# Optimization experiments

Measured on AMD Instinct MI355X. Metric: run time of the kernel, lower is better.

## Reference

```python
import jax, jax.numpy as jnp
import numpy as np
import math

B, L, C_IN = 64, 3168, 64
D_MODEL, K = 512, 16  # K = cycle_length (kernel width == stride)
W = L // K            # 198 output tokens from deform conv


def _positional(S, d, dtype):
    # PositionalEmbedding buffer, rows [0, S)
    pos = jnp.arange(S, dtype=jnp.float32)[:, None]
    div = jnp.exp(jnp.arange(0, d, 2, dtype=jnp.float32) * (-math.log(10000.0) / d))
    pe = jnp.zeros((S, d), jnp.float32)
    pe = pe.at[:, 0::2].set(jnp.sin(pos * div))
    pe = pe.at[:, 1::2].set(jnp.cos(pos * div))
    return pe.astype(dtype)


def setup_inputs() -> dict:
    key = jax.random.key(0)
    ks = jax.random.split(key, 6)
    fan_in = C_IN * K
    std = math.sqrt(2.0 / (1 + 0.01 ** 2) / fan_in)  # kaiming_normal, leaky_relu fan_in
    return {
        "x": jax.random.normal(ks[0], (B, L, C_IN), jnp.float32),
        "w_off": jax.random.normal(ks[1], (2 * K, C_IN, K), jnp.float32) * std,
        "b_off": jax.random.normal(ks[2], (2 * K,), jnp.float32) * 0.02,
        "w_def": jax.random.normal(ks[3], (D_MODEL, C_IN, K), jnp.float32) * std,
        "b_def": jax.random.normal(ks[4], (D_MODEL,), jnp.float32) * 0.02,
        "cls_token": jax.random.normal(ks[5], (1, 1, D_MODEL), jnp.float32),
    }


def _gather_cols(xt, idx, L_):
    # xt: (B, C, L); idx: (B, K, W) int32 -> (B, C, K, W), zero out-of-bounds
    b, c = xt.shape[0], xt.shape[1]
    valid = (idx >= 0) & (idx < L_)
    idxc = jnp.clip(idx, 0, L_ - 1).reshape(b, 1, -1)
    g = jnp.take_along_axis(xt, jnp.broadcast_to(idxc, (b, c, idxc.shape[-1])), axis=2)
    g = g.reshape(b, c, idx.shape[1], idx.shape[2])
    return jnp.where(valid[:, None], g, 0.0)


def reference(x, w_off, b_off, w_def, b_def, cls_token):
    b, l, c = x.shape
    w = l // K
    # offset conv: kernel (1,K), stride (1,K) == non-overlapping windows
    xr = x[:, : w * K, :].reshape(b, w, K, c)              # (B, W, K, C)
    off = jnp.einsum('bwkc,ock->bow', xr, w_off) + b_off[None, :, None]  # (B, 2K, W)
    dy = off[:, 0::2]                                      # (B, K, W)
    dx = off[:, 1::2]
    # sampling positions along width (height is size 1, base y = 0)
    base = (jnp.arange(w)[None, :] * K + jnp.arange(K)[:, None]).astype(x.dtype)  # (K, W)
    px = base[None] + dx                                   # (B, K, W)
    x0 = jnp.floor(px)
    frac = px - x0
    x0i = x0.astype(jnp.int32)
    xt = x.transpose(0, 2, 1)                              # (B, C, L)
    v0 = _gather_cols(xt, x0i, l)
    v1 = _gather_cols(xt, x0i + 1, l)
    wy = jnp.maximum(0.0, 1.0 - jnp.abs(dy))               # vertical bilinear weight on row 0
    val = wy[:, None] * ((1.0 - frac)[:, None] * v0 + frac[:, None] * v1)  # (B, C, K, W)
    out = jnp.einsum('bckw,dck->bwd', val, w_def) + b_def  # (B, W, d_model)
    tok = jnp.concatenate([jnp.broadcast_to(cls_token, (b, 1, D_MODEL)), out], axis=1)
    pe = _positional(w + 1, D_MODEL, tok.dtype)
    return tok + pe[None]
```

## Files before the change

### kernel.cpp

```cpp
#include <hip/hip_runtime.h>
#include <math.h>
#include <stdint.h>

#define NB 64
#define NL 3168
#define NC 64
#define ND 512
#define NK 16
#define NW 198
#define NM 12672
#define KD 1024

typedef __attribute__((ext_vector_type(8))) short bf8_t;
typedef __attribute__((ext_vector_type(4))) float f4_t;

typedef const unsigned int __attribute__((address_space(1)))* as1_u32p;
typedef unsigned int __attribute__((address_space(3)))* as3_u32p;

__device__ __forceinline__ void gl_lds16(const void* g, void* l) {
  __builtin_amdgcn_global_load_lds((as1_u32p)(uintptr_t)g,
                                   (as3_u32p)(unsigned int)(uintptr_t)l, 16, 0, 0);
}

__device__ __forceinline__ unsigned short f2bf(float f) {
  union { float f; unsigned u; } v; v.f = f;
  unsigned r = v.u + 0x7FFFu + ((v.u >> 16) & 1u);
  return (unsigned short)(r >> 16);
}

__global__ void prep_kernel(const float* __restrict__ w_off, const float* __restrict__ w_def,
                            const float* __restrict__ cls, unsigned short* __restrict__ wofft,
                            unsigned short* __restrict__ wdeft, float* __restrict__ pe,
                            float* __restrict__ out) {
  int id = blockIdx.x * 256 + threadIdx.x;
  if (id < 524288) {
    int d = id >> 10, kc = id & 1023, k = kc >> 6, c = kc & 63;
    wdeft[id] = f2bf(w_def[d * 1024 + c * 16 + k]);
    return;
  }
  id -= 524288;
  if (id < 32768) {
    int o = id >> 10, kc = id & 1023, k = kc >> 6, c = kc & 63;
    wofft[id] = f2bf(w_off[o * 1024 + c * 16 + k]);
    return;
  }
  id -= 32768;
  if (id < 101888) {
    int pos = id >> 9, d = id & 511;
    int i = d >> 1;
    float freq = expf((float)(2 * i) * (-9.210340371976184f / 512.0f));
    float arg = (float)pos * freq;
    pe[id] = (d & 1) ? cosf(arg) : sinf(arg);
    return;
  }
  id -= 101888;
  {
    int b = id >> 9, d = id & 511;
    out[(size_t)(b * 199) * 512 + d] = cls[d] + ((d & 1) ? 1.0f : 0.0f);
  }
}

__launch_bounds__(256)
__global__ void offgemm_kernel(const float* __restrict__ x, const unsigned short* __restrict__ wofft,
                               const float* __restrict__ b_off, float* __restrict__ off_ws) {
  __shared__ float partial[4][16][33];
  int tid = threadIdx.x;
  int lane = tid & 63, wid = tid >> 6;
  int r16 = lane & 15, kg = lane >> 4;
  int row0 = blockIdx.x * 16;

  f4_t acc[2] = {};
  const float* arow = x + (size_t)(row0 + r16) * KD + wid * 256;
  const unsigned short* bcol0 = wofft + r16 * KD + wid * 256;
  const unsigned short* bcol1 = wofft + (16 + r16) * KD + wid * 256;

#pragma unroll
  for (int ks = 0; ks < 8; ++ks) {
    int k0 = ks * 32 + kg * 8;
    float4 v0 = *(const float4*)(arow + k0);
    float4 v1 = *(const float4*)(arow + k0 + 4);
    bf8_t a;
    a[0] = (short)f2bf(v0.x); a[1] = (short)f2bf(v0.y);
    a[2] = (short)f2bf(v0.z); a[3] = (short)f2bf(v0.w);
    a[4] = (short)f2bf(v1.x); a[5] = (short)f2bf(v1.y);
    a[6] = (short)f2bf(v1.z); a[7] = (short)f2bf(v1.w);
    bf8_t b0 = *(const bf8_t*)(bcol0 + k0);
    bf8_t b1 = *(const bf8_t*)(bcol1 + k0);
    acc[0] = __builtin_amdgcn_mfma_f32_16x16x32_bf16(a, b0, acc[0], 0, 0, 0);
    acc[1] = __builtin_amdgcn_mfma_f32_16x16x32_bf16(a, b1, acc[1], 0, 0, 0);
  }
#pragma unroll
  for (int n = 0; n < 2; ++n)
#pragma unroll
    for (int r = 0; r < 4; ++r)
      partial[wid][kg * 4 + r][n * 16 + r16] = acc[n][r];
  __syncthreads();
#pragma unroll
  for (int i = 0; i < 2; ++i) {
    int idx = tid * 2 + i;
    int r = idx >> 5, o = idx & 31;
    float s = partial[0][r][o] + partial[1][r][o] + partial[2][r][o] + partial[3][r][o];
    off_ws[(row0 + r) * 32 + o] = s + b_off[o];
  }
}

__global__ void sample_kernel(const float* __restrict__ x, const float* __restrict__ off_ws,
                              unsigned short* __restrict__ val_ws) {
  int tid = threadIdx.x;
  int wid = tid >> 6, lane = tid & 63;
  int row = blockIdx.x * 4 + wid;
  int b = row / NW, w = row - b * NW;
  const float* xb = x + (size_t)b * (NL * NC);
  const float* offr = off_ws + row * 32;
  unsigned short* dst = val_ws + (size_t)row * KD;
#pragma unroll
  for (int k = 0; k < 16; ++k) {
    float dy = offr[2 * k], dx = offr[2 * k + 1];
    float wy = fmaxf(0.f, 1.f - fabsf(dy));
    float px = (float)(w * 16 + k) + dx;
    float x0f = floorf(px);
    float frac = px - x0f;
    int x0 = (int)x0f;
    float v0 = (x0 >= 0 && x0 < NL) ? xb[x0 * 64 + lane] : 0.f;
    float v1 = (x0 + 1 >= 0 && x0 + 1 < NL) ? xb[(x0 + 1) * 64 + lane] : 0.f;
    float val = wy * ((1.f - frac) * v0 + frac * v1);
    dst[k * 64 + lane] = f2bf(val);
  }
}

__launch_bounds__(256)
__global__ void gemm_kernel(const unsigned short* __restrict__ val_ws,
                            const unsigned short* __restrict__ wdeft,
                            const float* __restrict__ b_def, const float* __restrict__ pe,
                            float* __restrict__ out) {
  __shared__ unsigned short As[128 * 64];
  __shared__ unsigned short Bs[128 * 64];
  int tid = threadIdx.x;
  int mt = blockIdx.x, nt = blockIdx.y;
  int lane = tid & 63, wid = tid >> 6;
  int r16 = lane & 15, kg = lane >> 4;
  int wr = wid >> 1, wc = wid & 1;
  f4_t acc[4][4] = {};

  int r_st = lane >> 3;
  int j_st = lane & 7;
  const char* aBase = (const char*)val_ws + (size_t)mt * 128 * 2048;
  const char* bBase = (const char*)wdeft + (size_t)nt * 128 * 2048;

  for (int ks = 0; ks < 16; ++ks) {
    __syncthreads();
#pragma unroll
    for (int i = 0; i < 4; ++i) {
      int seg = wid * 4 + i;
      int r = seg * 8 + r_st;
      int src_off = ((j_st ^ (r & 7)) << 4);
      gl_lds16(aBase + (size_t)r * 2048 + ks * 128 + src_off, &As[seg * 512]);
      gl_lds16(bBase + (size_t)r * 2048 + ks * 128 + src_off, &Bs[seg * 512]);
    }
    __syncthreads();
#pragma unroll
    for (int jb = 0; jb < 8; jb += 4) {
      bf8_t af[4], bf[4];
#pragma unroll
      for (int m = 0; m < 4; ++m) {
        int R = wr * 64 + m * 16 + r16;
        af[m] = *(const bf8_t*)&As[R * 64 + (((jb + kg) ^ (R & 7)) << 3)];
      }
#pragma unroll
      for (int n = 0; n < 4; ++n) {
        int Rc = wc * 64 + n * 16 + r16;
        bf[n] = *(const bf8_t*)&Bs[Rc * 64 + (((jb + kg) ^ (Rc & 7)) << 3)];
      }
#pragma unroll
      for (int m = 0; m < 4; ++m)
#pragma unroll
        for (int n = 0; n < 4; ++n)
          acc[m][n] = __builtin_amdgcn_mfma_f32_16x16x32_bf16(af[m], bf[n], acc[m][n], 0, 0, 0);
    }
  }
#pragma unroll
  for (int m = 0; m < 4; ++m)
#pragma unroll
    for (int n = 0; n < 4; ++n)
#pragma unroll
      for (int r = 0; r < 4; ++r) {
        int grow = mt * 128 + wr * 64 + m * 16 + kg * 4 + r;
        int gcol = nt * 128 + wc * 64 + n * 16 + r16;
        int bi = grow / NW, wi = grow - bi * NW;
        out[((size_t)(bi * 199 + wi + 1)) * 512 + gcol] =
            acc[m][n][r] + b_def[gcol] + pe[(wi + 1) * 512 + gcol];
      }
}

extern "C" void kernel_launch(void* const* d_in, const int* in_sizes, int n_in,
                              void* d_out, int out_size, void* d_ws, size_t ws_size,
                              hipStream_t stream) {
  const float* x     = (const float*)d_in[0];
  const float* w_off = (const float*)d_in[1];
  const float* b_off = (const float*)d_in[2];
  const float* w_def = (const float*)d_in[3];
  const float* b_def = (const float*)d_in[4];
  const float* cls   = (const float*)d_in[5];
  float* out = (float*)d_out;
  char* ws = (char*)d_ws;
  unsigned short* val_ws = (unsigned short*)ws;
  unsigned short* wofft  = (unsigned short*)(ws + 25952256);
  unsigned short* wdeft  = (unsigned short*)(ws + 26017792);
  float* pe              = (float*)(ws + 27066368);
  float* off_ws          = (float*)(ws + 27473920);

  prep_kernel<<<2702, 256, 0, stream>>>(w_off, w_def, cls, wofft, wdeft, pe, out);
  offgemm_kernel<<<NM / 16, 256, 0, stream>>>(x, wofft, b_off, off_ws);
  sample_kernel<<<NM / 4, 256, 0, stream>>>(x, off_ws, val_ws);
  gemm_kernel<<<dim3(99, 4), 256, 0, stream>>>(val_ws, wdeft, b_def, pe, out);
}
```

Baseline: 68.28 us.

## Fuse offset GEMM with sampling, switch val layout to c-major, double-buffer GEMM

Merges the offset-conv GEMM and the bilinear sampling into one kernel. Offsets stay in shared memory instead of taking a round trip through global memory, and one launch is removed. Each lane now writes its 16 k-values contiguously with vector stores, so val and w_def use a (c,k) K-ordering and w_def can be converted without a transpose. The main GEMM gains double-buffered LDS staging with one barrier per step, so loads overlap MFMA work. The cost is fewer sampling threads per block and twice the LDS, which may lower occupancy.

```diff
diff --git a/kernel.cpp b/kernel.cpp
--- a/kernel.cpp
+++ b/kernel.cpp
@@ -34,8 +34,7 @@
                             float* __restrict__ out) {
   int id = blockIdx.x * 256 + threadIdx.x;
   if (id < 524288) {
-    int d = id >> 10, kc = id & 1023, k = kc >> 6, c = kc & 63;
-    wdeft[id] = f2bf(w_def[d * 1024 + c * 16 + k]);
+    wdeft[id] = f2bf(w_def[id]);
     return;
   }
   id -= 524288;
@@ -61,9 +60,12 @@
 }
 
 __launch_bounds__(256)
-__global__ void offgemm_kernel(const float* __restrict__ x, const unsigned short* __restrict__ wofft,
-                               const float* __restrict__ b_off, float* __restrict__ off_ws) {
+__global__ void offsample_kernel(const float* __restrict__ x,
+                                 const unsigned short* __restrict__ wofft,
+                                 const float* __restrict__ b_off,
+                                 unsigned short* __restrict__ val_ws) {
   __shared__ float partial[4][16][33];
+  __shared__ float offs[16][32];
   int tid = threadIdx.x;
   int lane = tid & 63, wid = tid >> 6;
   int r16 = lane & 15, kg = lane >> 4;
@@ -99,32 +101,37 @@
   for (int i = 0; i < 2; ++i) {
     int idx = tid * 2 + i;
     int r = idx >> 5, o = idx & 31;
-    float s = partial[0][r][o] + partial[1][r][o] + partial[2][r][o] + partial[3][r][o];
-    off_ws[(row0 + r) * 32 + o] = s + b_off[o];
-  }
-}
-
-__global__ void sample_kernel(const float* __restrict__ x, const float* __restrict__ off_ws,
-                              unsigned short* __restrict__ val_ws) {
-  int tid = threadIdx.x;
-  int wid = tid >> 6, lane = tid & 63;
-  int row = blockIdx.x * 4 + wid;
-  int b = row / NW, w = row - b * NW;
-  const float* xb = x + (size_t)b * (NL * NC);
-  const float* offr = off_ws + row * 32;
-  unsigned short* dst = val_ws + (size_t)row * KD;
-#pragma unroll
-  for (int k = 0; k < 16; ++k) {
-    float dy = offr[2 * k], dx = offr[2 * k + 1];
-    float wy = fmaxf(0.f, 1.f - fabsf(dy));
-    float px = (float)(w * 16 + k) + dx;
-    float x0f = floorf(px);
-    float frac = px - x0f;
-    int x0 = (int)x0f;
-    float v0 = (x0 >= 0 && x0 < NL) ? xb[x0 * 64 + lane] : 0.f;
-    float v1 = (x0 + 1 >= 0 && x0 + 1 < NL) ? xb[(x0 + 1) * 64 + lane] : 0.f;
-    float val = wy * ((1.f - frac) * v0 + frac * v1);
-    dst[k * 64 + lane] = f2bf(val);
+    offs[r][o] = partial[0][r][o] + partial[1][r][o] + partial[2][r][o] + partial[3][r][o]
+                 + b_off[o];
+  }
+  __syncthreads();
+
+#pragma unroll
+  for (int rr = 0; rr < 4; ++rr) {
+    int rp = wid * 4 + rr;
+    int rg = row0 + rp;
+    int b = rg / NW, w = rg - b * NW;
+    const float* xb = x + (size_t)b * (NL * NC);
+    unsigned short vv[16];
+#pragma unroll
+    for (int k = 0; k < 16; ++k) {
+      float dy = offs[rp][2 * k], dx = offs[rp][2 * k + 1];
+      float wy = fmaxf(0.f, 1.f - fabsf(dy));
+      float px = (float)(w * 16 + k) + dx;
+      float x0f = floorf(px);
+      float frac = px - x0f;
+      int x0 = (int)x0f;
+      float v0 = (x0 >= 0 && x0 < NL) ? xb[x0 * 64 + lane] : 0.f;
+      float v1 = (x0 + 1 >= 0 && x0 + 1 < NL) ? xb[(x0 + 1) * 64 + lane] : 0.f;
+      vv[k] = f2bf(wy * ((1.f - frac) * v0 + frac * v1));
+    }
+    unsigned int p[8];
+#pragma unroll
+    for (int i = 0; i < 8; ++i)
+      p[i] = (unsigned int)vv[2 * i] | ((unsigned int)vv[2 * i + 1] << 16);
+    uint4* dst = (uint4*)(val_ws + (size_t)rg * KD + lane * 16);
+    dst[0] = make_uint4(p[0], p[1], p[2], p[3]);
+    dst[1] = make_uint4(p[4], p[5], p[6], p[7]);
   }
 }
 
@@ -133,8 +140,8 @@
                             const unsigned short* __restrict__ wdeft,
                             const float* __restrict__ b_def, const float* __restrict__ pe,
                             float* __restrict__ out) {
-  __shared__ unsigned short As[128 * 64];
-  __shared__ unsigned short Bs[128 * 64];
+  __shared__ unsigned short As[2][128 * 64];
+  __shared__ unsigned short Bs[2][128 * 64];
   int tid = threadIdx.x;
   int mt = blockIdx.x, nt = blockIdx.y;
   int lane = tid & 63, wid = tid >> 6;
@@ -147,29 +154,30 @@
   const char* aBase = (const char*)val_ws + (size_t)mt * 128 * 2048;
   const char* bBase = (const char*)wdeft + (size_t)nt * 128 * 2048;
 
-  for (int ks = 0; ks < 16; ++ks) {
-    __syncthreads();
+  auto STAGE = [&](int ks, int buf) {
 #pragma unroll
     for (int i = 0; i < 4; ++i) {
       int seg = wid * 4 + i;
       int r = seg * 8 + r_st;
       int src_off = ((j_st ^ (r & 7)) << 4);
-      gl_lds16(aBase + (size_t)r * 2048 + ks * 128 + src_off, &As[seg * 512]);
-      gl_lds16(bBase + (size_t)r * 2048 + ks * 128 + src_off, &Bs[seg * 512]);
+      gl_lds16(aBase + (size_t)r * 2048 + ks * 128 + src_off, &As[buf][seg * 512]);
+      gl_lds16(bBase + (size_t)r * 2048 + ks * 128 + src_off, &Bs[buf][seg * 512]);
     }
-    __syncthreads();
+  };
+
+  auto COMPUTE = [&](int buf) {
 #pragma unroll
     for (int jb = 0; jb < 8; jb += 4) {
       bf8_t af[4], bf[4];
 #pragma unroll
       for (int m = 0; m < 4; ++m) {
         int R = wr * 64 + m * 16 + r16;
-        af[m] = *(const bf8_t*)&As[R * 64 + (((jb + kg) ^ (R & 7)) << 3)];
+        af[m] = *(const bf8_t*)&As[buf][R * 64 + (((jb + kg) ^ (R & 7)) << 3)];
       }
 #pragma unroll
       for (int n = 0; n < 4; ++n) {
         int Rc = wc * 64 + n * 16 + r16;
-        bf[n] = *(const bf8_t*)&Bs[Rc * 64 + (((jb + kg) ^ (Rc & 7)) << 3)];
+        bf[n] = *(const bf8_t*)&Bs[buf][Rc * 64 + (((jb + kg) ^ (Rc & 7)) << 3)];
       }
 #pragma unroll
       for (int m = 0; m < 4; ++m)
@@ -177,7 +185,18 @@
         for (int n = 0; n < 4; ++n)
           acc[m][n] = __builtin_amdgcn_mfma_f32_16x16x32_bf16(af[m], bf[n], acc[m][n], 0, 0, 0);
     }
-  }
+  };
+
+  STAGE(0, 0);
+  __syncthreads();
+#pragma unroll
+  for (int ks = 0; ks < 15; ++ks) {
+    STAGE(ks + 1, (ks + 1) & 1);
+    COMPUTE(ks & 1);
+    __syncthreads();
+  }
+  COMPUTE(1);
+
 #pragma unroll
   for (int m = 0; m < 4; ++m)
 #pragma unroll
@@ -207,10 +226,8 @@
   unsigned short* wofft  = (unsigned short*)(ws + 25952256);
   unsigned short* wdeft  = (unsigned short*)(ws + 26017792);
   float* pe              = (float*)(ws + 27066368);
-  float* off_ws          = (float*)(ws + 27473920);
 
   prep_kernel<<<2702, 256, 0, stream>>>(w_off, w_def, cls, wofft, wdeft, pe, out);
-  offgemm_kernel<<<NM / 16, 256, 0, stream>>>(x, wofft, b_off, off_ws);
-  sample_kernel<<<NM / 4, 256, 0, stream>>>(x, off_ws, val_ws);
+  offsample_kernel<<<NM / 16, 256, 0, stream>>>(x, wofft, b_off, val_ws);
   gemm_kernel<<<dim3(99, 4), 256, 0, stream>>>(val_ws, wdeft, b_def, pe, out);
 }
```

New measurement: 70.09 us. 2.7% more time.
